# Optimization experiments

Measured on AMD Instinct MI355X. Metric: run time of the kernel, lower is better.

The kernel has to match this reference:

```python
import jax, jax.numpy as jnp
import numpy as np

T_STEPS = 4
TAU = 2.0
EPS = 1e-5
NUM_HEADS = 8
SCALE = 0.125  # hardcoded self.scale in the torch module
SG_ALPHA = 4.0  # spikingjelly default sigmoid surrogate alpha


@jax.custom_vjp
def heaviside(x):
    return (x >= 0.0).astype(x.dtype)

def _hv_fwd(x):
    return heaviside(x), x

def _hv_bwd(x, g):
    s = jax.nn.sigmoid(SG_ALPHA * x)
    return (g * SG_ALPHA * s * (1.0 - s),)

heaviside.defvjp(_hv_fwd, _hv_bwd)


def lif(x_seq, v_th):
    # MultiStepLIFNode: v += (x - v)/tau; spike = H(v - v_th); hard reset to 0 (detached).
    def step(v, x):
        v = v + (x - v) / TAU
        s = heaviside(v - v_th)
        v = v * (1.0 - jax.lax.stop_gradient(s))
        return v, s
    _, out = jax.lax.scan(step, jnp.zeros_like(x_seq[0]), x_seq)
    return out


def bn(x, g, b):
    # BatchNorm1d training-mode stats over (batch, length) per channel; x: (TB, C, N)
    m = jnp.mean(x, axis=(0, 2), keepdims=True)
    var = jnp.mean((x - m) ** 2, axis=(0, 2), keepdims=True)
    return g[None, :, None] * (x - m) * jax.lax.rsqrt(var + EPS) + b[None, :, None]


def _branch(x, w, b, g, beta):
    # linear over channel dim + BN + LIF, then split heads -> (T,B,H,N,d)
    T, B, C, N = x.shape
    y = jnp.einsum('oc,tbcn->tbon', w, x) + b[None, None, :, None]
    y = bn(y.reshape(T * B, C, N), g, beta).reshape(T, B, C, N)
    y = lif(y, 1.0)
    d = C // NUM_HEADS
    return y.transpose(0, 1, 3, 2).reshape(T, B, N, NUM_HEADS, d).transpose(0, 1, 3, 2, 4)


def setup_inputs() -> dict:
    key = jax.random.key(0)
    ks = jax.random.split(key, 6)
    B, C, N = 8, 512, 1024
    bound = float(np.sqrt(6.0 / (3 * C + C)))  # xavier_uniform for (3C, C)
    return {
        'q': jax.random.normal(ks[0], (B, C, N), jnp.float32),
        'k': jax.random.normal(ks[1], (B, C, N), jnp.float32),
        'v': jax.random.normal(ks[2], (B, C, N), jnp.float32),
        'in_proj_w': jax.random.uniform(ks[3], (3 * C, C), jnp.float32, -bound, bound),
        'in_proj_b': jnp.zeros((3 * C,), jnp.float32),
        'q_gamma': jnp.ones((C,), jnp.float32),
        'q_beta': jnp.zeros((C,), jnp.float32),
        'k_gamma': jnp.ones((C,), jnp.float32),
        'k_beta': jnp.zeros((C,), jnp.float32),
        'v_gamma': jnp.ones((C,), jnp.float32),
        'v_beta': jnp.zeros((C,), jnp.float32),
        'proj_w': jax.random.normal(ks[4], (C, C), jnp.float32) * (1.0 / np.sqrt(C)),
        'proj_b': jnp.zeros((C,), jnp.float32),
        'p_gamma': jnp.ones((C,), jnp.float32),
        'p_beta': jnp.zeros((C,), jnp.float32),
    }


def reference(q, k, v, in_proj_w, in_proj_b, q_gamma, q_beta, k_gamma, k_beta,
              v_gamma, v_beta, proj_w, proj_b, p_gamma, p_beta):
    B, C, N = q.shape
    qs = jnp.broadcast_to(q[None], (T_STEPS, B, C, N))
    ks_ = jnp.broadcast_to(k[None], (T_STEPS, B, C, N))
    vs = jnp.broadcast_to(v[None], (T_STEPS, B, C, N))

    qh = _branch(qs, in_proj_w[:C], in_proj_b[:C], q_gamma, q_beta)        # (T,B,H,N,d)
    kh = _branch(ks_, in_proj_w[C:2 * C], in_proj_b[C:2 * C], k_gamma, k_beta)
    vh = _branch(vs, in_proj_w[2 * C:], in_proj_b[2 * C:], v_gamma, v_beta)

    # linear attention: (k^T v) then q @ (k^T v)
    ktv = jnp.einsum('tbhnd,tbhne->tbhde', kh, vh)            # (T,B,H,d,d)
    att = jnp.einsum('tbhnd,tbhde->tbhne', qh, ktv) * SCALE   # (T,B,H,N,d)

    x = att.transpose(0, 1, 2, 4, 3).reshape(T_STEPS, B, C, N)
    x = lif(x, 0.5)  # attn_lif with v_threshold=0.5

    z = jnp.einsum('oc,tbcn->tbon', proj_w, x) + proj_b[None, None, :, None]  # 1x1 conv
    z = bn(z.reshape(T_STEPS * B, C, N), p_gamma, p_beta).reshape(T_STEPS, B, C, N)
    return lif(z, 1.0)
```

## Files before the change

### kernel.cpp

```cpp
#include <hip/hip_runtime.h>

#define C    512
#define NDIM 1024
#define BDIM 8
#define TDIM 4
#define HDIM 8
#define CN   (C*NDIM)
#define BCN  (BDIM*CN)

typedef unsigned short u16;
typedef unsigned int   u32;
typedef unsigned long long u64;
typedef __attribute__((ext_vector_type(8))) short bf8v;
typedef __attribute__((ext_vector_type(4))) float f4v;

__device__ __forceinline__ u16 f2bf(float f) {
    u32 u = __float_as_uint(f);
    u32 r = u + 0x7FFFu + ((u >> 16) & 1u);
    return (u16)(r >> 16);
}
__device__ __forceinline__ float bf2f(u16 h) { return __uint_as_float((u32)h << 16); }

#if defined(__has_builtin)
#if __has_builtin(__builtin_amdgcn_global_load_lds)
#define HAS_GLL 1
#endif
#endif
#ifdef HAS_GLL
#define GLD(gp, lp) __builtin_amdgcn_global_load_lds( \
    (const __attribute__((address_space(1))) u32*)(gp), \
    (__attribute__((address_space(3))) u32*)(lp), 16, 0, 0)
#else
#define GLD(gp, lp) (*(uint4*)(lp) = *(const uint4*)(const void*)(gp))
#endif

__global__ __launch_bounds__(256) void gemm_in3_k(
    const float* __restrict__ W, const float* __restrict__ bias,
    const float* __restrict__ Xq, const float* __restrict__ Xk,
    const float* __restrict__ Xv, float* __restrict__ Y3)
{
    __shared__ float As[16][132];
    __shared__ float Bs[16][132];
    const int tid = threadIdx.x;
    const int bz = blockIdx.z;
    const int br = bz >> 3, b = bz & 7;
    const int m0 = blockIdx.y * 128;
    const int n0 = blockIdx.x * 128;
    const float* Xb = (br == 0 ? Xq : (br == 1 ? Xk : Xv)) + (size_t)b * CN;
    const int rowOff = br * 512;

    const int ra = tid >> 2, ka = (tid & 3) * 4;
    const int kb = tid >> 5, nb = (tid & 31) * 4;
    const int tx = tid & 15, ty = tid >> 4;

    float acc[2][2][4][4];
    #pragma unroll
    for (int mq = 0; mq < 2; mq++)
        #pragma unroll
        for (int nq = 0; nq < 2; nq++)
            #pragma unroll
            for (int i = 0; i < 4; i++)
                #pragma unroll
                for (int j = 0; j < 4; j++) acc[mq][nq][i][j] = 0.f;

    for (int k0 = 0; k0 < 512; k0 += 16) {
        float4 a0 = *(const float4*)&W[(size_t)(rowOff + m0 + ra) * 512 + k0 + ka];
        float4 a1 = *(const float4*)&W[(size_t)(rowOff + m0 + 64 + ra) * 512 + k0 + ka];
        float4 b0 = *(const float4*)&Xb[(size_t)(k0 + kb) * NDIM + n0 + nb];
        float4 b1 = *(const float4*)&Xb[(size_t)(k0 + 8 + kb) * NDIM + n0 + nb];
        __syncthreads();
        As[ka + 0][ra] = a0.x; As[ka + 1][ra] = a0.y;
        As[ka + 2][ra] = a0.z; As[ka + 3][ra] = a0.w;
        As[ka + 0][64 + ra] = a1.x; As[ka + 1][64 + ra] = a1.y;
        As[ka + 2][64 + ra] = a1.z; As[ka + 3][64 + ra] = a1.w;
        *(float4*)&Bs[kb][nb]     = b0;
        *(float4*)&Bs[kb + 8][nb] = b1;
        __syncthreads();
        #pragma unroll
        for (int k = 0; k < 16; k++) {
            float av[2][4], bv[2][4];
            *(float4*)av[0] = *(const float4*)&As[k][ty * 4];
            *(float4*)av[1] = *(const float4*)&As[k][64 + ty * 4];
            *(float4*)bv[0] = *(const float4*)&Bs[k][tx * 4];
            *(float4*)bv[1] = *(const float4*)&Bs[k][64 + tx * 4];
            #pragma unroll
            for (int mq = 0; mq < 2; mq++)
                #pragma unroll
                for (int nq = 0; nq < 2; nq++)
                    #pragma unroll
                    for (int i = 0; i < 4; i++)
                        #pragma unroll
                        for (int j = 0; j < 4; j++)
                            acc[mq][nq][i][j] += av[mq][i] * bv[nq][j];
        }
    }
    #pragma unroll
    for (int mq = 0; mq < 2; mq++)
        #pragma unroll
        for (int i = 0; i < 4; i++) {
            const int mrow = mq * 64 + ty * 4 + i;
            float bsv = bias[rowOff + m0 + mrow];
            float* yr = Y3 + (size_t)bz * CN + (size_t)(m0 + mrow) * NDIM + n0;
            #pragma unroll
            for (int nq = 0; nq < 2; nq++) {
                float4 o4 = make_float4(acc[mq][nq][i][0] + bsv, acc[mq][nq][i][1] + bsv,
                                        acc[mq][nq][i][2] + bsv, acc[mq][nq][i][3] + bsv);
                *(float4*)&yr[nq * 64 + tx * 4] = o4;
            }
        }
}

__global__ __launch_bounds__(256) void split_pw_k(
    const float* __restrict__ PW, u16* __restrict__ Ps)
{
    const int idx = blockIdx.x * 256 + threadIdx.x;
    float x = PW[idx];
    u16 h1 = f2bf(x); float r1 = x - bf2f(h1);
    u16 h2 = f2bf(r1); float r2 = r1 - bf2f(h2);
    u16 h3 = f2bf(r2);
    Ps[idx] = h1; Ps[idx + 262144] = h2; Ps[idx + 2 * 262144] = h3;
}

__global__ __launch_bounds__(256, 2) void gemm_proj_mfma(
    const u16* __restrict__ Ps, const unsigned char* __restrict__ spkT,
    float* __restrict__ Z)
{
    __shared__ __align__(16) u16 Ab[2][12288];
    __shared__ __align__(16) u16 Bb[2][4096];
    const int tid = threadIdx.x;
    const int zb = blockIdx.z, t = zb >> 3, bb = zb & 7;
    const int m0 = blockIdx.y * 128, n0 = blockIdx.x * 128;

    u32 aoff[2][3];
    int lofs[2];
    #pragma unroll
    for (int r = 0; r < 2; r++) {
        const int cid = tid + (r << 8);
        const int mm = cid & 15, kg = (cid >> 4) & 3, mt = cid >> 6;
        lofs[r] = cid * 8;
        #pragma unroll
        for (int s = 0; s < 3; s++)
            aoff[r][s] = (u32)s * 262144u + (u32)(m0 + mt * 16 + mm) * 512u + kg * 8;
    }
    auto stageA = [&](int ki2, int p2) {
        const u32 kk = (u32)ki2 << 5;
        #pragma unroll
        for (int r = 0; r < 2; r++)
            #pragma unroll
            for (int s = 0; s < 3; s++)
                GLD(Ps + aoff[r][s] + kk, &Ab[p2][s * 4096 + lofs[r]]);
    };
    const int nn = tid & 15, ntl = (tid >> 4) & 7, seg = tid >> 7;
    const u32 srcB = ((u32)bb * 1024u + (u32)(n0 + ntl * 16 + nn)) * 512u + seg * 16;
    const int ldsB0 = (ntl * 64 + seg * 32 + nn) * 8;
    auto convB = [&](uint4 braw, int p2) {
        u32 bs[4] = {braw.x, braw.y, braw.z, braw.w};
        u32 w[8];
        #pragma unroll
        for (int qq = 0; qq < 4; qq++) {
            u32 v = bs[qq] >> t;
            w[qq * 2 + 0] = ((v & 1u) ? 0x3F80u : 0u) | ((v & 0x100u) ? 0x3F800000u : 0u);
            w[qq * 2 + 1] = (((v >> 16) & 1u) ? 0x3F80u : 0u) | ((v & 0x1000000u) ? 0x3F800000u : 0u);
        }
        *(uint4*)&Bb[p2][ldsB0]       = make_uint4(w[0], w[1], w[2], w[3]);
        *(uint4*)&Bb[p2][ldsB0 + 128] = make_uint4(w[4], w[5], w[6], w[7]);
    };

    const int lane = tid & 63, wv = tid >> 6;
    const int wm = wv >> 1, wn = wv & 1;
    const int q = lane >> 4, ln = lane & 15;
    int afo[4], bfo[4];
    #pragma unroll
    for (int i = 0; i < 4; i++) {
        afo[i] = ((wm * 4 + i) * 64 + q * 16 + ln) * 8;
        bfo[i] = ((wn * 4 + i) * 64 + q * 16 + ln) * 8;
    }

    f4v acc[4][4];
    #pragma unroll
    for (int i = 0; i < 4; i++)
        #pragma unroll
        for (int j = 0; j < 4; j++) acc[i][j] = (f4v){0.f, 0.f, 0.f, 0.f};

    stageA(0, 0);
    convB(*(const uint4*)&spkT[srcB], 0);
    uint4 braw;
    for (int ki = 0; ki < 16; ki++) {
        const int p = ki & 1;
        __syncthreads();
        if (ki < 15) {
            stageA(ki + 1, p ^ 1);
            braw = *(const uint4*)&spkT[srcB + ((u32)(ki + 1) << 5)];
        }
        bf8v bf[4];
        #pragma unroll
        for (int j = 0; j < 4; j++) bf[j] = *(const bf8v*)&Bb[p][bfo[j]];
        #pragma unroll
        for (int sa = 0; sa < 3; sa++) {
            bf8v af[4];
            #pragma unroll
            for (int i = 0; i < 4; i++) af[i] = *(const bf8v*)&Ab[p][sa * 4096 + afo[i]];
            #pragma unroll
            for (int i = 0; i < 4; i++)
                #pragma unroll
                for (int j = 0; j < 4; j++)
                    acc[i][j] = __builtin_amdgcn_mfma_f32_16x16x32_bf16(af[i], bf[j], acc[i][j], 0, 0, 0);
        }
        if (ki < 15) convB(braw, p ^ 1);
    }
    float* Zb = Z + (size_t)zb * CN;
    #pragma unroll
    for (int i = 0; i < 4; i++) {
        const int row = m0 + (wm * 4 + i) * 16 + q * 4;
        #pragma unroll
        for (int g = 0; g < 4; g++) {
            float* zr = Zb + (size_t)(row + g) * 1024 + n0 + ln;
            #pragma unroll
            for (int j = 0; j < 4; j++)
                zr[(wn * 4 + j) * 16] = acc[i][j][g];
        }
    }
}

__global__ __launch_bounds__(256) void chan_sum3_k(
    const float* __restrict__ X3, float* __restrict__ mean3, int outer)
{
    __shared__ float red[256];
    const int gb = blockIdx.x;
    const int o = gb & (C - 1);
    const float* X = X3 + (size_t)(gb >> 9) * BCN;
    const int tid = threadIdx.x;
    const int total = outer * NDIM;
    float s = 0.f;
    for (int i = tid; i < total; i += 256) {
        int ou = i >> 10, n = i & 1023;
        s += X[(size_t)(ou * C + o) * NDIM + n];
    }
    red[tid] = s; __syncthreads();
    for (int off = 128; off > 0; off >>= 1) {
        if (tid < off) red[tid] += red[tid + off];
        __syncthreads();
    }
    if (tid == 0) mean3[gb] = red[0] / (float)total;
}

__global__ __launch_bounds__(256) void chan_var3_k(
    const float* __restrict__ X3, const float* __restrict__ mean3,
    float* __restrict__ rstd3, int outer)
{
    __shared__ float red[256];
    const int gb = blockIdx.x;
    const int o = gb & (C - 1);
    const float* X = X3 + (size_t)(gb >> 9) * BCN;
    const int tid = threadIdx.x;
    const int total = outer * NDIM;
    const float m = mean3[gb];
    float s = 0.f;
    for (int i = tid; i < total; i += 256) {
        int ou = i >> 10, n = i & 1023;
        float d = X[(size_t)(ou * C + o) * NDIM + n] - m;
        s += d * d;
    }
    red[tid] = s; __syncthreads();
    for (int off = 128; off > 0; off >>= 1) {
        if (tid < off) red[tid] += red[tid + off];
        __syncthreads();
    }
    if (tid == 0) rstd3[gb] = 1.f / sqrtf(red[0] / (float)total + 1e-5f);
}

__global__ __launch_bounds__(256) void bn_lif_pack_k(
    const float* __restrict__ Y, const float* __restrict__ mean,
    const float* __restrict__ rstd, const float* __restrict__ gamma,
    const float* __restrict__ beta, unsigned char* __restrict__ spk)
{
    const int idx = blockIdx.x * 256 + threadIdx.x;
    const int o = (idx >> 10) & (C - 1);
    float y = Y[idx];
    float x = gamma[o] * (y - mean[o]);
    x = x * rstd[o] + beta[o];
    float v = 0.f; unsigned bits = 0;
    #pragma unroll
    for (int t = 0; t < 4; t++) {
        v += (x - v) * 0.5f;
        if (v - 1.0f >= 0.f) { bits |= (1u << t); v = 0.f; }
    }
    spk[idx] = (unsigned char)bits;
}

__global__ __launch_bounds__(256) void bn_lif_kv_k(
    const float* __restrict__ Y, const float* __restrict__ mean,
    const float* __restrict__ rstd, const float* __restrict__ gamma,
    const float* __restrict__ beta, u64* __restrict__ bits)
{
    const int idx = blockIdx.x * 256 + threadIdx.x;
    const int o = (idx >> 10) & (C - 1);
    const int b = idx >> 19;
    const int n = idx & 1023;
    float y = Y[idx];
    float x = gamma[o] * (y - mean[o]);
    x = x * rstd[o] + beta[o];
    float v = 0.f; unsigned sb = 0;
    #pragma unroll
    for (int t = 0; t < 4; t++) {
        v += (x - v) * 0.5f;
        if (v - 1.0f >= 0.f) { sb |= (1u << t); v = 0.f; }
    }
    const int lane = threadIdx.x & 63;
    #pragma unroll
    for (int t = 0; t < 4; t++) {
        u64 m = __ballot((sb >> t) & 1);
        if (lane == t)
            bits[((size_t)(t * BDIM + b) * C + o) * 16 + (n >> 6)] = m;
    }
}

__global__ __launch_bounds__(256) void qpack_k(
    const unsigned char* __restrict__ spk, u64* __restrict__ qm)
{
    __shared__ unsigned char tile[64][80];
    const int tid = threadIdx.x;
    const int bh = blockIdx.x; const int h = bh & 7, b = bh >> 3;
    const int n0 = blockIdx.y * 64;
    {
        int dd = tid >> 2, sg = tid & 3;
        *(uint4*)&tile[dd][sg * 16] =
            *(const uint4*)&spk[(size_t)(b * C + h * 64 + dd) * NDIM + n0 + sg * 16];
    }
    __syncthreads();
    const int lane = tid & 63, wv = tid >> 6;
    for (int i = 0; i < 16; i++) {
        int j = wv * 16 + i;
        unsigned s = tile[lane][j];
        #pragma unroll
        for (int t = 0; t < 4; t++) {
            u64 m = __ballot((s >> t) & 1);
            if (lane == t)
                qm[(size_t)((t * BDIM + b) * HDIM + h) * NDIM + n0 + j] = m;
        }
    }
}

__global__ __launch_bounds__(256) void ktv_k(
    const u64* __restrict__ kb, const u64* __restrict__ vb,
    u16* __restrict__ ktv)
{
    __shared__ u64 ks[64][17];
    __shared__ u64 vs[64][17];
    const int tid = threadIdx.x;
    const int g = blockIdx.x;
    const int h = g & 7, b = (g >> 3) & 7, t = g >> 6;
    const size_t base = ((size_t)(t * BDIM + b) * C + h * 64) * 16;
    {
        int r = tid >> 2, w0 = (tid & 3) * 4;
        #pragma unroll
        for (int j = 0; j < 4; j++) {
            ks[r][w0 + j] = kb[base + r * 16 + w0 + j];
            vs[r][w0 + j] = vb[base + r * 16 + w0 + j];
        }
    }
    __syncthreads();
    const int dd = tid >> 2, e0 = (tid & 3) * 16;
    u64 kr[16];
    #pragma unroll
    for (int w = 0; w < 16; w++) kr[w] = ks[dd][w];
    #pragma unroll
    for (int i = 0; i < 16; i++) {
        int e = e0 + i;
        int s = 0;
        #pragma unroll
        for (int w = 0; w < 16; w++) s += __popcll(kr[w] & vs[e][w]);
        ktv[(size_t)(g * 64 + dd) * 64 + e] = (u16)s;
    }
}

__global__ __launch_bounds__(256) void att_lif_k(
    const u16* __restrict__ ktv, const u64* __restrict__ qm,
    unsigned char* __restrict__ spkT)
{
    __shared__ u16 ks[4][64][64];
    const int tid = threadIdx.x;
    const int bh = blockIdx.x; const int h = bh & 7, b = bh >> 3;
    const int n0 = blockIdx.y * 64;
    #pragma unroll
    for (int t = 0; t < 4; t++) {
        const u32* src = (const u32*)&ktv[(size_t)((t * BDIM + b) * HDIM + h) * 4096];
        u32* dst = (u32*)&ks[t][0][0];
        #pragma unroll
        for (int j = 0; j < 8; j++) dst[tid + 256 * j] = src[tid + 256 * j];
    }
    __syncthreads();
    const int lane = tid & 63, wv = tid >> 6;
    for (int i = 0; i < 16; i++) {
        const int n = n0 + wv * 16 + i;
        float v = 0.f; unsigned bits = 0;
        #pragma unroll
        for (int t = 0; t < 4; t++) {
            u64 m = qm[(size_t)((t * BDIM + b) * HDIM + h) * NDIM + n];
            int acc = 0;
            while (m) {
                int dd = __ffsll(m) - 1;
                m &= m - 1;
                acc += ks[t][dd][lane];
            }
            float x = (float)acc * 0.125f;
            v += (x - v) * 0.5f;
            if (v - 0.5f >= 0.f) { bits |= (1u << t); v = 0.f; }
        }
        spkT[((size_t)b * 1024 + n) * 512 + h * 64 + lane] = (unsigned char)bits;
    }
}

__global__ __launch_bounds__(256) void final_bn_lif_k(
    float* __restrict__ Z, const float* __restrict__ mean,
    const float* __restrict__ rstd, const float* __restrict__ gamma,
    const float* __restrict__ beta)
{
    const int idx = blockIdx.x * 256 + threadIdx.x;
    const int o = (idx >> 10) & (C - 1);
    const float m = mean[o], rs = rstd[o], g = gamma[o], bt = beta[o];
    float v = 0.f;
    float outs[4];
    #pragma unroll
    for (int t = 0; t < 4; t++) {
        float z = Z[(size_t)t * BCN + idx];
        float x = g * (z - m);
        x = x * rs + bt;
        v += (x - v) * 0.5f;
        float s = (v - 1.0f >= 0.f) ? 1.f : 0.f;
        v *= (1.f - s);
        outs[t] = s;
    }
    #pragma unroll
    for (int t = 0; t < 4; t++) Z[(size_t)t * BCN + idx] = outs[t];
}

extern "C" void kernel_launch(void* const* d_in, const int* in_sizes, int n_in,
                              void* d_out, int out_size, void* d_ws, size_t ws_size,
                              hipStream_t stream)
{
    const float* q     = (const float*)d_in[0];
    const float* k     = (const float*)d_in[1];
    const float* v     = (const float*)d_in[2];
    const float* W     = (const float*)d_in[3];
    const float* Wb    = (const float*)d_in[4];
    const float* qg    = (const float*)d_in[5];
    const float* qb    = (const float*)d_in[6];
    const float* kg    = (const float*)d_in[7];
    const float* kbt   = (const float*)d_in[8];
    const float* vg    = (const float*)d_in[9];
    const float* vbt   = (const float*)d_in[10];
    const float* pw    = (const float*)d_in[11];
    const float* pg    = (const float*)d_in[13];
    const float* pbeta = (const float*)d_in[14];

    char* p = (char*)d_ws;
    unsigned char* spk = (unsigned char*)p; p += (size_t)BCN;
    u64* qmv = (u64*)p;                     p += (size_t)TDIM * BDIM * HDIM * NDIM * 8;
    u64* kbits = (u64*)p;                   p += (size_t)TDIM * BDIM * C * 16 * 8;
    u64* vbits = (u64*)p;                   p += (size_t)TDIM * BDIM * C * 16 * 8;
    u16* ktv = (u16*)p;                     p += (size_t)TDIM * BDIM * HDIM * 64 * 64 * 2;
    float* mean3 = (float*)p;               p += 8192;
    float* rstd3 = (float*)p;               p += 8192;

    float* Y3 = (float*)d_out;
    float* outF = (float*)d_out;
    u16* Ps = (u16*)qmv;
    unsigned char* spkT = spk;

    const float* Gs[3] = {qg, kg, vg};
    const float* Bt[3] = {qb, kbt, vbt};

    gemm_in3_k<<<dim3(8, 4, 24), 256, 0, stream>>>(W, Wb, q, k, v, Y3);
    chan_sum3_k<<<3 * C, 256, 0, stream>>>(Y3, mean3, BDIM);
    chan_var3_k<<<3 * C, 256, 0, stream>>>(Y3, mean3, rstd3, BDIM);
    for (int br = 0; br < 3; ++br) {
        if (br == 0) {
            bn_lif_pack_k<<<BCN / 256, 256, 0, stream>>>(Y3,
                mean3, rstd3, Gs[0], Bt[0], spk);
            qpack_k<<<dim3(64, 16), 256, 0, stream>>>(spk, qmv);
        } else {
            bn_lif_kv_k<<<BCN / 256, 256, 0, stream>>>(Y3 + (size_t)br * BCN,
                mean3 + br * C, rstd3 + br * C, Gs[br], Bt[br],
                br == 1 ? kbits : vbits);
        }
    }
    ktv_k<<<256, 256, 0, stream>>>(kbits, vbits, ktv);
    att_lif_k<<<dim3(64, 16), 256, 0, stream>>>(ktv, qmv, spkT);
    split_pw_k<<<1024, 256, 0, stream>>>(pw, Ps);
    gemm_proj_mfma<<<dim3(8, 4, 32), 256, 0, stream>>>(Ps, spkT, outF);
    chan_sum3_k<<<C, 256, 0, stream>>>(outF, mean3, TDIM * BDIM);
    chan_var3_k<<<C, 256, 0, stream>>>(outF, mean3, rstd3, TDIM * BDIM);
    final_bn_lif_k<<<BCN / 256, 256, 0, stream>>>(outF, mean3, rstd3, pg, pbeta);
}
```

Baseline: 553.4 us.

## Double-buffer input GEMM and fuse stats, spike packing and attention kernels

The input-projection GEMM now double-buffers its LDS tiles and loads B directly into LDS, overlapping the next tile's fetch with compute. Mean and variance kernels are merged into one two-pass kernel. The q/k/v BN+LIF spike packing and the weight split are combined into one multi-role launch, and ktv is computed inside the attention kernel, so the intermediate spike buffer and ktv round trips go away. In exchange, each attention block recomputes k^T v for its head, which duplicates popcount work across the 16 n-tiles.

```diff
diff --git a/kernel.cpp b/kernel.cpp
--- a/kernel.cpp
+++ b/kernel.cpp
@@ -39,8 +39,8 @@
     const float* __restrict__ Xq, const float* __restrict__ Xk,
     const float* __restrict__ Xv, float* __restrict__ Y3)
 {
-    __shared__ float As[16][132];
-    __shared__ float Bs[16][132];
+    __shared__ float As[2][16][132];
+    __shared__ __align__(16) float Bs[2][16][128];
     const int tid = threadIdx.x;
     const int bz = blockIdx.z;
     const int br = bz >> 3, b = bz & 7;
@@ -50,8 +50,13 @@
     const int rowOff = br * 512;
 
     const int ra = tid >> 2, ka = (tid & 3) * 4;
-    const int kb = tid >> 5, nb = (tid & 31) * 4;
+    const int bk = tid >> 5, bn = (tid & 31) * 4;
     const int tx = tid & 15, ty = tid >> 4;
+
+    const float* wA0 = &W[(size_t)(rowOff + m0 + ra) * 512 + ka];
+    const float* wA1 = &W[(size_t)(rowOff + m0 + 64 + ra) * 512 + ka];
+    const float* xB0 = &Xb[(size_t)bk * NDIM + n0 + bn];
+    const float* xB1 = &Xb[(size_t)(bk + 8) * NDIM + n0 + bn];
 
     float acc[2][2][4][4];
     #pragma unroll
@@ -63,26 +68,35 @@
                 #pragma unroll
                 for (int j = 0; j < 4; j++) acc[mq][nq][i][j] = 0.f;
 
+    {
+        float4 a0 = *(const float4*)wA0;
+        float4 a1 = *(const float4*)wA1;
+        GLD(xB0, &Bs[0][bk][bn]);
+        GLD(xB1, &Bs[0][bk + 8][bn]);
+        As[0][ka + 0][ra] = a0.x; As[0][ka + 1][ra] = a0.y;
+        As[0][ka + 2][ra] = a0.z; As[0][ka + 3][ra] = a0.w;
+        As[0][ka + 0][64 + ra] = a1.x; As[0][ka + 1][64 + ra] = a1.y;
+        As[0][ka + 2][64 + ra] = a1.z; As[0][ka + 3][64 + ra] = a1.w;
+    }
+    __syncthreads();
+
     for (int k0 = 0; k0 < 512; k0 += 16) {
-        float4 a0 = *(const float4*)&W[(size_t)(rowOff + m0 + ra) * 512 + k0 + ka];
-        float4 a1 = *(const float4*)&W[(size_t)(rowOff + m0 + 64 + ra) * 512 + k0 + ka];
-        float4 b0 = *(const float4*)&Xb[(size_t)(k0 + kb) * NDIM + n0 + nb];
-        float4 b1 = *(const float4*)&Xb[(size_t)(k0 + 8 + kb) * NDIM + n0 + nb];
-        __syncthreads();
-        As[ka + 0][ra] = a0.x; As[ka + 1][ra] = a0.y;
-        As[ka + 2][ra] = a0.z; As[ka + 3][ra] = a0.w;
-        As[ka + 0][64 + ra] = a1.x; As[ka + 1][64 + ra] = a1.y;
-        As[ka + 2][64 + ra] = a1.z; As[ka + 3][64 + ra] = a1.w;
-        *(float4*)&Bs[kb][nb]     = b0;
-        *(float4*)&Bs[kb + 8][nb] = b1;
-        __syncthreads();
+        const int p = (k0 >> 4) & 1;
+        const bool more = (k0 < 496);
+        float4 na0, na1;
+        if (more) {
+            na0 = *(const float4*)(wA0 + k0 + 16);
+            na1 = *(const float4*)(wA1 + k0 + 16);
+            GLD(xB0 + (size_t)(k0 + 16) * NDIM, &Bs[p ^ 1][bk][bn]);
+            GLD(xB1 + (size_t)(k0 + 16) * NDIM, &Bs[p ^ 1][bk + 8][bn]);
+        }
         #pragma unroll
         for (int k = 0; k < 16; k++) {
             float av[2][4], bv[2][4];
-            *(float4*)av[0] = *(const float4*)&As[k][ty * 4];
-            *(float4*)av[1] = *(const float4*)&As[k][64 + ty * 4];
-            *(float4*)bv[0] = *(const float4*)&Bs[k][tx * 4];
-            *(float4*)bv[1] = *(const float4*)&Bs[k][64 + tx * 4];
+            *(float4*)av[0] = *(const float4*)&As[p][k][ty * 4];
+            *(float4*)av[1] = *(const float4*)&As[p][k][64 + ty * 4];
+            *(float4*)bv[0] = *(const float4*)&Bs[p][k][tx * 4];
+            *(float4*)bv[1] = *(const float4*)&Bs[p][k][64 + tx * 4];
             #pragma unroll
             for (int mq = 0; mq < 2; mq++)
                 #pragma unroll
@@ -93,6 +107,13 @@
                         for (int j = 0; j < 4; j++)
                             acc[mq][nq][i][j] += av[mq][i] * bv[nq][j];
         }
+        if (more) {
+            As[p ^ 1][ka + 0][ra] = na0.x; As[p ^ 1][ka + 1][ra] = na0.y;
+            As[p ^ 1][ka + 2][ra] = na0.z; As[p ^ 1][ka + 3][ra] = na0.w;
+            As[p ^ 1][ka + 0][64 + ra] = na1.x; As[p ^ 1][ka + 1][64 + ra] = na1.y;
+            As[p ^ 1][ka + 2][64 + ra] = na1.z; As[p ^ 1][ka + 3][64 + ra] = na1.w;
+        }
+        __syncthreads();
     }
     #pragma unroll
     for (int mq = 0; mq < 2; mq++)
@@ -110,15 +131,191 @@
         }
 }
 
-__global__ __launch_bounds__(256) void split_pw_k(
-    const float* __restrict__ PW, u16* __restrict__ Ps)
-{
-    const int idx = blockIdx.x * 256 + threadIdx.x;
-    float x = PW[idx];
-    u16 h1 = f2bf(x); float r1 = x - bf2f(h1);
-    u16 h2 = f2bf(r1); float r2 = r1 - bf2f(h2);
-    u16 h3 = f2bf(r2);
-    Ps[idx] = h1; Ps[idx + 262144] = h2; Ps[idx + 2 * 262144] = h3;
+__global__ __launch_bounds__(256) void chan_stats2_k(
+    const float* __restrict__ X3, float* __restrict__ mean3,
+    float* __restrict__ rstd3, int outer)
+{
+    __shared__ float red[256];
+    __shared__ float m_sh;
+    const int gb = blockIdx.x;
+    const int o = gb & (C - 1);
+    const float* X = X3 + (size_t)(gb >> 9) * BCN;
+    const int tid = threadIdx.x;
+    const int total = outer * NDIM;
+    float s = 0.f;
+    for (int i = tid; i < total; i += 256) {
+        int ou = i >> 10, n = i & 1023;
+        s += X[(size_t)(ou * C + o) * NDIM + n];
+    }
+    red[tid] = s; __syncthreads();
+    for (int off = 128; off > 0; off >>= 1) {
+        if (tid < off) red[tid] += red[tid + off];
+        __syncthreads();
+    }
+    if (tid == 0) { float m = red[0] / (float)total; mean3[gb] = m; m_sh = m; }
+    __syncthreads();
+    const float m = m_sh;
+    float s2 = 0.f;
+    for (int i = tid; i < total; i += 256) {
+        int ou = i >> 10, n = i & 1023;
+        float d = X[(size_t)(ou * C + o) * NDIM + n] - m;
+        s2 += d * d;
+    }
+    red[tid] = s2; __syncthreads();
+    for (int off = 128; off > 0; off >>= 1) {
+        if (tid < off) red[tid] += red[tid + off];
+        __syncthreads();
+    }
+    if (tid == 0) rstd3[gb] = 1.f / sqrtf(red[0] / (float)total + 1e-5f);
+}
+
+__global__ __launch_bounds__(256) void spikes_k(
+    const float* __restrict__ Y3, const float* __restrict__ mean3,
+    const float* __restrict__ rstd3,
+    const float* __restrict__ qg, const float* __restrict__ qb,
+    const float* __restrict__ kg, const float* __restrict__ kbt,
+    const float* __restrict__ vg, const float* __restrict__ vbt,
+    const float* __restrict__ PW,
+    u64* __restrict__ qm, u64* __restrict__ kbits, u64* __restrict__ vbits,
+    u16* __restrict__ Ps)
+{
+    __shared__ unsigned char tile[64][68];
+    const int tid = threadIdx.x;
+    const int bid = blockIdx.x;
+    if (bid < 1024) {
+        const int b = bid >> 7, h = (bid >> 4) & 7, nt = bid & 15;
+        const int c_l = tid >> 2, sg = (tid & 3) * 16;
+        const int o = h * 64 + c_l;
+        const float m = mean3[o], rs = rstd3[o], g = qg[o], bt = qb[o];
+        const float* Yr = Y3 + ((size_t)b * C + o) * NDIM + nt * 64 + sg;
+        #pragma unroll
+        for (int j = 0; j < 4; j++) {
+            float4 y4 = *(const float4*)&Yr[j * 4];
+            float ys[4] = {y4.x, y4.y, y4.z, y4.w};
+            #pragma unroll
+            for (int e = 0; e < 4; e++) {
+                float x = g * (ys[e] - m);
+                x = x * rs + bt;
+                float v = 0.f; unsigned bits = 0;
+                #pragma unroll
+                for (int t = 0; t < 4; t++) {
+                    v += (x - v) * 0.5f;
+                    if (v - 1.0f >= 0.f) { bits |= (1u << t); v = 0.f; }
+                }
+                tile[c_l][sg + j * 4 + e] = (unsigned char)bits;
+            }
+        }
+        __syncthreads();
+        const int lane = tid & 63, wv = tid >> 6;
+        #pragma unroll
+        for (int i = 0; i < 16; i++) {
+            const int nl = wv * 16 + i;
+            unsigned s = tile[lane][nl];
+            #pragma unroll
+            for (int t = 0; t < 4; t++) {
+                u64 mk = __ballot((s >> t) & 1);
+                if (lane == t)
+                    qm[(size_t)((t * BDIM + b) * HDIM + h) * NDIM + nt * 64 + nl] = mk;
+            }
+        }
+    } else if (bid < 3072) {
+        const int r = bid - 1024;
+        const int br = r >> 10;
+        const int rr = r & 1023;
+        const int b = rr >> 7, ct = (rr >> 4) & 7, nt = rr & 15;
+        const float* Yb = Y3 + (size_t)(br + 1) * BCN + (size_t)b * CN;
+        const float* mean = mean3 + (br + 1) * C;
+        const float* rstd = rstd3 + (br + 1) * C;
+        const float* gam = br == 0 ? kg : vg;
+        const float* bet = br == 0 ? kbt : vbt;
+        u64* bits = br == 0 ? kbits : vbits;
+        const int lane = tid & 63, wv = tid >> 6;
+        #pragma unroll
+        for (int i = 0; i < 16; i++) {
+            const int o = ct * 64 + wv * 16 + i;
+            const float m = mean[o], rs = rstd[o], g = gam[o], bt = bet[o];
+            float y = Yb[(size_t)o * NDIM + nt * 64 + lane];
+            float x = g * (y - m);
+            x = x * rs + bt;
+            float v = 0.f; unsigned sb = 0;
+            #pragma unroll
+            for (int t = 0; t < 4; t++) {
+                v += (x - v) * 0.5f;
+                if (v - 1.0f >= 0.f) { sb |= (1u << t); v = 0.f; }
+            }
+            #pragma unroll
+            for (int t = 0; t < 4; t++) {
+                u64 mk = __ballot((sb >> t) & 1);
+                if (lane == t)
+                    bits[((size_t)(t * BDIM + b) * C + o) * 16 + nt] = mk;
+            }
+        }
+    } else {
+        const int idx = (bid - 3072) * 256 + tid;
+        float x = PW[idx];
+        u16 h1 = f2bf(x); float r1 = x - bf2f(h1);
+        u16 h2 = f2bf(r1); float r2 = r1 - bf2f(h2);
+        u16 h3 = f2bf(r2);
+        Ps[idx] = h1; Ps[idx + 262144] = h2; Ps[idx + 2 * 262144] = h3;
+    }
+}
+
+__global__ __launch_bounds__(256) void att_ktv_k(
+    const u64* __restrict__ kb, const u64* __restrict__ vb,
+    const u64* __restrict__ qm, unsigned char* __restrict__ spkT)
+{
+    __shared__ u16 ks[4][64][64];
+    __shared__ u64 kst[64][17];
+    __shared__ u64 vst[64][17];
+    const int tid = threadIdx.x;
+    const int bh = blockIdx.x; const int h = bh & 7, b = bh >> 3;
+    const int n0 = blockIdx.y * 64;
+    for (int t = 0; t < 4; t++) {
+        const size_t base = ((size_t)(t * BDIM + b) * C + h * 64) * 16;
+        {
+            int r = tid >> 2, w0 = (tid & 3) * 4;
+            #pragma unroll
+            for (int j = 0; j < 4; j++) {
+                kst[r][w0 + j] = kb[base + r * 16 + w0 + j];
+                vst[r][w0 + j] = vb[base + r * 16 + w0 + j];
+            }
+        }
+        __syncthreads();
+        {
+            const int dd = tid >> 2, e0 = (tid & 3) * 16;
+            u64 kr[16];
+            #pragma unroll
+            for (int w = 0; w < 16; w++) kr[w] = kst[dd][w];
+            #pragma unroll
+            for (int i = 0; i < 16; i++) {
+                int e = e0 + i;
+                int s = 0;
+                #pragma unroll
+                for (int w = 0; w < 16; w++) s += __popcll(kr[w] & vst[e][w]);
+                ks[t][dd][e] = (u16)s;
+            }
+        }
+        __syncthreads();
+    }
+    const int lane = tid & 63, wv = tid >> 6;
+    for (int i = 0; i < 16; i++) {
+        const int n = n0 + wv * 16 + i;
+        float v = 0.f; unsigned bits = 0;
+        #pragma unroll
+        for (int t = 0; t < 4; t++) {
+            u64 m = qm[(size_t)((t * BDIM + b) * HDIM + h) * NDIM + n];
+            int acc = 0;
+            while (m) {
+                int dd = __ffsll(m) - 1;
+                m &= m - 1;
+                acc += ks[t][dd][lane];
+            }
+            float x = (float)acc * 0.125f;
+            v += (x - v) * 0.5f;
+            if (v - 0.5f >= 0.f) { bits |= (1u << t); v = 0.f; }
+        }
+        spkT[((size_t)b * 1024 + n) * 512 + h * 64 + lane] = (unsigned char)bits;
+    }
 }
 
 __global__ __launch_bounds__(256, 2) void gemm_proj_mfma(
@@ -219,195 +416,6 @@
             for (int j = 0; j < 4; j++)
                 zr[(wn * 4 + j) * 16] = acc[i][j][g];
         }
-    }
-}
-
-__global__ __launch_bounds__(256) void chan_sum3_k(
-    const float* __restrict__ X3, float* __restrict__ mean3, int outer)
-{
-    __shared__ float red[256];
-    const int gb = blockIdx.x;
-    const int o = gb & (C - 1);
-    const float* X = X3 + (size_t)(gb >> 9) * BCN;
-    const int tid = threadIdx.x;
-    const int total = outer * NDIM;
-    float s = 0.f;
-    for (int i = tid; i < total; i += 256) {
-        int ou = i >> 10, n = i & 1023;
-        s += X[(size_t)(ou * C + o) * NDIM + n];
-    }
-    red[tid] = s; __syncthreads();
-    for (int off = 128; off > 0; off >>= 1) {
-        if (tid < off) red[tid] += red[tid + off];
-        __syncthreads();
-    }
-    if (tid == 0) mean3[gb] = red[0] / (float)total;
-}
-
-__global__ __launch_bounds__(256) void chan_var3_k(
-    const float* __restrict__ X3, const float* __restrict__ mean3,
-    float* __restrict__ rstd3, int outer)
-{
-    __shared__ float red[256];
-    const int gb = blockIdx.x;
-    const int o = gb & (C - 1);
-    const float* X = X3 + (size_t)(gb >> 9) * BCN;
-    const int tid = threadIdx.x;
-    const int total = outer * NDIM;
-    const float m = mean3[gb];
-    float s = 0.f;
-    for (int i = tid; i < total; i += 256) {
-        int ou = i >> 10, n = i & 1023;
-        float d = X[(size_t)(ou * C + o) * NDIM + n] - m;
-        s += d * d;
-    }
-    red[tid] = s; __syncthreads();
-    for (int off = 128; off > 0; off >>= 1) {
-        if (tid < off) red[tid] += red[tid + off];
-        __syncthreads();
-    }
-    if (tid == 0) rstd3[gb] = 1.f / sqrtf(red[0] / (float)total + 1e-5f);
-}
-
-__global__ __launch_bounds__(256) void bn_lif_pack_k(
-    const float* __restrict__ Y, const float* __restrict__ mean,
-    const float* __restrict__ rstd, const float* __restrict__ gamma,
-    const float* __restrict__ beta, unsigned char* __restrict__ spk)
-{
-    const int idx = blockIdx.x * 256 + threadIdx.x;
-    const int o = (idx >> 10) & (C - 1);
-    float y = Y[idx];
-    float x = gamma[o] * (y - mean[o]);
-    x = x * rstd[o] + beta[o];
-    float v = 0.f; unsigned bits = 0;
-    #pragma unroll
-    for (int t = 0; t < 4; t++) {
-        v += (x - v) * 0.5f;
-        if (v - 1.0f >= 0.f) { bits |= (1u << t); v = 0.f; }
-    }
-    spk[idx] = (unsigned char)bits;
-}
-
-__global__ __launch_bounds__(256) void bn_lif_kv_k(
-    const float* __restrict__ Y, const float* __restrict__ mean,
-    const float* __restrict__ rstd, const float* __restrict__ gamma,
-    const float* __restrict__ beta, u64* __restrict__ bits)
-{
-    const int idx = blockIdx.x * 256 + threadIdx.x;
-    const int o = (idx >> 10) & (C - 1);
-    const int b = idx >> 19;
-    const int n = idx & 1023;
-    float y = Y[idx];
-    float x = gamma[o] * (y - mean[o]);
-    x = x * rstd[o] + beta[o];
-    float v = 0.f; unsigned sb = 0;
-    #pragma unroll
-    for (int t = 0; t < 4; t++) {
-        v += (x - v) * 0.5f;
-        if (v - 1.0f >= 0.f) { sb |= (1u << t); v = 0.f; }
-    }
-    const int lane = threadIdx.x & 63;
-    #pragma unroll
-    for (int t = 0; t < 4; t++) {
-        u64 m = __ballot((sb >> t) & 1);
-        if (lane == t)
-            bits[((size_t)(t * BDIM + b) * C + o) * 16 + (n >> 6)] = m;
-    }
-}
-
-__global__ __launch_bounds__(256) void qpack_k(
-    const unsigned char* __restrict__ spk, u64* __restrict__ qm)
-{
-    __shared__ unsigned char tile[64][80];
-    const int tid = threadIdx.x;
-    const int bh = blockIdx.x; const int h = bh & 7, b = bh >> 3;
-    const int n0 = blockIdx.y * 64;
-    {
-        int dd = tid >> 2, sg = tid & 3;
-        *(uint4*)&tile[dd][sg * 16] =
-            *(const uint4*)&spk[(size_t)(b * C + h * 64 + dd) * NDIM + n0 + sg * 16];
-    }
-    __syncthreads();
-    const int lane = tid & 63, wv = tid >> 6;
-    for (int i = 0; i < 16; i++) {
-        int j = wv * 16 + i;
-        unsigned s = tile[lane][j];
-        #pragma unroll
-        for (int t = 0; t < 4; t++) {
-            u64 m = __ballot((s >> t) & 1);
-            if (lane == t)
-                qm[(size_t)((t * BDIM + b) * HDIM + h) * NDIM + n0 + j] = m;
-        }
-    }
-}
-
-__global__ __launch_bounds__(256) void ktv_k(
-    const u64* __restrict__ kb, const u64* __restrict__ vb,
-    u16* __restrict__ ktv)
-{
-    __shared__ u64 ks[64][17];
-    __shared__ u64 vs[64][17];
-    const int tid = threadIdx.x;
-    const int g = blockIdx.x;
-    const int h = g & 7, b = (g >> 3) & 7, t = g >> 6;
-    const size_t base = ((size_t)(t * BDIM + b) * C + h * 64) * 16;
-    {
-        int r = tid >> 2, w0 = (tid & 3) * 4;
-        #pragma unroll
-        for (int j = 0; j < 4; j++) {
-            ks[r][w0 + j] = kb[base + r * 16 + w0 + j];
-            vs[r][w0 + j] = vb[base + r * 16 + w0 + j];
-        }
-    }
-    __syncthreads();
-    const int dd = tid >> 2, e0 = (tid & 3) * 16;
-    u64 kr[16];
-    #pragma unroll
-    for (int w = 0; w < 16; w++) kr[w] = ks[dd][w];
-    #pragma unroll
-    for (int i = 0; i < 16; i++) {
-        int e = e0 + i;
-        int s = 0;
-        #pragma unroll
-        for (int w = 0; w < 16; w++) s += __popcll(kr[w] & vs[e][w]);
-        ktv[(size_t)(g * 64 + dd) * 64 + e] = (u16)s;
-    }
-}
-
-__global__ __launch_bounds__(256) void att_lif_k(
-    const u16* __restrict__ ktv, const u64* __restrict__ qm,
-    unsigned char* __restrict__ spkT)
-{
-    __shared__ u16 ks[4][64][64];
-    const int tid = threadIdx.x;
-    const int bh = blockIdx.x; const int h = bh & 7, b = bh >> 3;
-    const int n0 = blockIdx.y * 64;
-    #pragma unroll
-    for (int t = 0; t < 4; t++) {
-        const u32* src = (const u32*)&ktv[(size_t)((t * BDIM + b) * HDIM + h) * 4096];
-        u32* dst = (u32*)&ks[t][0][0];
-        #pragma unroll
-        for (int j = 0; j < 8; j++) dst[tid + 256 * j] = src[tid + 256 * j];
-    }
-    __syncthreads();
-    const int lane = tid & 63, wv = tid >> 6;
-    for (int i = 0; i < 16; i++) {
-        const int n = n0 + wv * 16 + i;
-        float v = 0.f; unsigned bits = 0;
-        #pragma unroll
-        for (int t = 0; t < 4; t++) {
-            u64 m = qm[(size_t)((t * BDIM + b) * HDIM + h) * NDIM + n];
-            int acc = 0;
-            while (m) {
-                int dd = __ffsll(m) - 1;
-                m &= m - 1;
-                acc += ks[t][dd][lane];
-            }
-            float x = (float)acc * 0.125f;
-            v += (x - v) * 0.5f;
-            if (v - 0.5f >= 0.f) { bits |= (1u << t); v = 0.f; }
-        }
-        spkT[((size_t)b * 1024 + n) * 512 + h * 64 + lane] = (unsigned char)bits;
     }
 }
 
@@ -455,41 +463,23 @@
     const float* pbeta = (const float*)d_in[14];
 
     char* p = (char*)d_ws;
-    unsigned char* spk = (unsigned char*)p; p += (size_t)BCN;
     u64* qmv = (u64*)p;                     p += (size_t)TDIM * BDIM * HDIM * NDIM * 8;
     u64* kbits = (u64*)p;                   p += (size_t)TDIM * BDIM * C * 16 * 8;
     u64* vbits = (u64*)p;                   p += (size_t)TDIM * BDIM * C * 16 * 8;
-    u16* ktv = (u16*)p;                     p += (size_t)TDIM * BDIM * HDIM * 64 * 64 * 2;
+    u16* Ps = (u16*)p;                      p += (size_t)3 * 262144 * 2;
+    unsigned char* spkT = (unsigned char*)p; p += (size_t)BCN;
     float* mean3 = (float*)p;               p += 8192;
     float* rstd3 = (float*)p;               p += 8192;
 
     float* Y3 = (float*)d_out;
     float* outF = (float*)d_out;
-    u16* Ps = (u16*)qmv;
-    unsigned char* spkT = spk;
-
-    const float* Gs[3] = {qg, kg, vg};
-    const float* Bt[3] = {qb, kbt, vbt};
 
     gemm_in3_k<<<dim3(8, 4, 24), 256, 0, stream>>>(W, Wb, q, k, v, Y3);
-    chan_sum3_k<<<3 * C, 256, 0, stream>>>(Y3, mean3, BDIM);
-    chan_var3_k<<<3 * C, 256, 0, stream>>>(Y3, mean3, rstd3, BDIM);
-    for (int br = 0; br < 3; ++br) {
-        if (br == 0) {
-            bn_lif_pack_k<<<BCN / 256, 256, 0, stream>>>(Y3,
-                mean3, rstd3, Gs[0], Bt[0], spk);
-            qpack_k<<<dim3(64, 16), 256, 0, stream>>>(spk, qmv);
-        } else {
-            bn_lif_kv_k<<<BCN / 256, 256, 0, stream>>>(Y3 + (size_t)br * BCN,
-                mean3 + br * C, rstd3 + br * C, Gs[br], Bt[br],
-                br == 1 ? kbits : vbits);
-        }
-    }
-    ktv_k<<<256, 256, 0, stream>>>(kbits, vbits, ktv);
-    att_lif_k<<<dim3(64, 16), 256, 0, stream>>>(ktv, qmv, spkT);
-    split_pw_k<<<1024, 256, 0, stream>>>(pw, Ps);
+    chan_stats2_k<<<3 * C, 256, 0, stream>>>(Y3, mean3, rstd3, BDIM);
+    spikes_k<<<4096, 256, 0, stream>>>(Y3, mean3, rstd3, qg, qb, kg, kbt, vg, vbt,
+                                       pw, qmv, kbits, vbits, Ps);
+    att_ktv_k<<<dim3(64, 16), 256, 0, stream>>>(kbits, vbits, qmv, spkT);
     gemm_proj_mfma<<<dim3(8, 4, 32), 256, 0, stream>>>(Ps, spkT, outF);
-    chan_sum3_k<<<C, 256, 0, stream>>>(outF, mean3, TDIM * BDIM);
-    chan_var3_k<<<C, 256, 0, stream>>>(outF, mean3, rstd3, TDIM * BDIM);
+    chan_stats2_k<<<C, 256, 0, stream>>>(outF, mean3, rstd3, TDIM * BDIM);
     final_bn_lif_k<<<BCN / 256, 256, 0, stream>>>(outF, mean3, rstd3, pg, pbeta);
 }
```

Measured after the change: 741.4 us. +34.0%, slower.
